# Kernel optimization log

Measured on AMD Instinct MI355X. Metric: run time of the kernel, lower is better.

The kernel has to match this reference:

```python
import jax, jax.numpy as jnp
import numpy as np

B, LQ, LK, D, NH = 16, 1024, 1024, 160, 8
HD = D // NH
EPS = 1e-5


def _ln(x, g, b):
    m = x.mean(-1, keepdims=True)
    v = ((x - m) ** 2).mean(-1, keepdims=True)
    return (x - m) / jnp.sqrt(v + EPS) * g + b


def _heads(x, L):
    # [B,L,D] -> [B,NH,L,HD]
    return x.reshape(B, L, NH, HD).transpose(0, 2, 1, 3)


def _attn(qh, kh, vh, scale):
    logits = jnp.einsum('bhqd,bhkd->bhqk', qh, kh) * scale
    p = jax.nn.softmax(logits, axis=-1)
    o = jnp.einsum('bhqk,bhkd->bhqd', p, vh)
    return o.transpose(0, 2, 1, 3).reshape(B, -1, D)


def setup_inputs() -> dict:
    key = jax.random.key(0)
    ks = jax.random.split(key, 16)
    s = 0.02
    inp = {
        'q': jax.random.normal(ks[0], (B, LQ, D), jnp.float32),
        'kv': jax.random.normal(ks[1], (B, LK, D), jnp.float32),
        'ln1_g': jnp.ones((D,), jnp.float32), 'ln1_b': jnp.zeros((D,), jnp.float32),
        'sa_in_w': jax.random.normal(ks[2], (3 * D, D), jnp.float32) * s,
        'sa_in_b': jnp.zeros((3 * D,), jnp.float32),
        'sa_out_w': jax.random.normal(ks[3], (D, D), jnp.float32) * s,
        'sa_out_b': jnp.zeros((D,), jnp.float32),
        'ln2_g': jnp.ones((D,), jnp.float32), 'ln2_b': jnp.zeros((D,), jnp.float32),
        'lnkv_g': jnp.ones((D,), jnp.float32), 'lnkv_b': jnp.zeros((D,), jnp.float32),
        'ca_qw': jax.random.normal(ks[4], (D, D), jnp.float32) * s,
        'ca_qb': jnp.zeros((D,), jnp.float32),
        'ca_kw': jax.random.normal(ks[5], (D, D), jnp.float32) * s,
        'ca_kb': jnp.zeros((D,), jnp.float32),
        'ca_vw': jax.random.normal(ks[6], (D, D), jnp.float32) * s,
        'ca_vb': jnp.zeros((D,), jnp.float32),
        'ca_ow': jax.random.normal(ks[7], (D, D), jnp.float32) * s,
        'ca_ob': jnp.zeros((D,), jnp.float32),
        'log_tau': jnp.zeros((1,), jnp.float32),
        'lnf_g': jnp.ones((D,), jnp.float32), 'lnf_b': jnp.zeros((D,), jnp.float32),
        'w1': jax.random.normal(ks[8], (4 * D, D), jnp.float32) * s,
        'b1': jnp.zeros((4 * D,), jnp.float32),
        'w2': jax.random.normal(ks[9], (D, 4 * D), jnp.float32) * s,
        'b2': jnp.zeros((D,), jnp.float32),
    }
    return inp


def reference(q, kv, ln1_g, ln1_b, sa_in_w, sa_in_b, sa_out_w, sa_out_b,
              ln2_g, ln2_b, lnkv_g, lnkv_b, ca_qw, ca_qb, ca_kw, ca_kb,
              ca_vw, ca_vb, ca_ow, ca_ob, log_tau, lnf_g, lnf_b,
              w1, b1, w2, b2):
    # --- self-attention (pre-LN), standard 1/sqrt(hd) scale ---
    qn = _ln(q, ln1_g, ln1_b)
    qkv = qn @ sa_in_w.T + sa_in_b  # [B,LQ,3D]
    sq, sk, sv = jnp.split(qkv, 3, axis=-1)
    sa = _attn(_heads(sq, LQ), _heads(sk, LQ), _heads(sv, LQ), HD ** -0.5)
    sa = sa @ sa_out_w.T + sa_out_b
    q = q + sa  # DropPath is identity in eval

    # --- cross-attention with learnable temperature ---
    qn = _ln(q, ln2_g, ln2_b)
    kvn = _ln(kv, lnkv_g, lnkv_b)
    tau = jnp.minimum(jax.nn.softplus(log_tau) + 0.5, 2.0)  # clamp max=2.0
    scale = (HD ** -0.5) / tau[0]
    qh = _heads(qn @ ca_qw.T + ca_qb, LQ)
    kh = _heads(kvn @ ca_kw.T + ca_kb, LK)
    vh = _heads(kvn @ ca_vw.T + ca_vb, LK)
    ca = _attn(qh, kh, vh, scale) @ ca_ow.T + ca_ob
    q = q + ca

    # --- FFN with exact GELU ---
    h = _ln(q, lnf_g, lnf_b) @ w1.T + b1
    h = jax.nn.gelu(h, approximate=False)
    q = q + (h @ w2.T + b2)
    return q
```

## Files before the change

### kernel.cpp

```cpp
#include <hip/hip_runtime.h>
#include <hip/hip_bf16.h>
#include <math.h>

#define LQN 1024
#define LKN 1024
#define NB 16
#define DM 160
#define NHEADS 8
#define HDIM 20

typedef __attribute__((ext_vector_type(8))) short bf16x8;
typedef __attribute__((ext_vector_type(4))) float f32x4;

__device__ __forceinline__ float bf2f(unsigned short h) {
  union { unsigned int u; float f; } c; c.u = ((unsigned int)h) << 16; return c.f;
}
__device__ __forceinline__ unsigned short f2bf(float f) {
  union { float f; unsigned int u; } c; c.f = f;
  unsigned int lsb = (c.u >> 16) & 1u;
  unsigned int r = c.u + 0x7fffu + lsb;
  return (unsigned short)(r >> 16);
}
__device__ __forceinline__ unsigned int cvtpk(float a, float b) {
  unsigned int r;
  asm("v_cvt_pk_bf16_f32 %0, %1, %2" : "=v"(r) : "v"(a), "v"(b));
  return r;
}
__device__ __forceinline__ float ex2(float x) { return __builtin_amdgcn_exp2f(x); }

__global__ void zero_kernel(uint4* __restrict__ p, int n4) {
  int i = blockIdx.x * 256 + threadIdx.x;
  if (i < n4) p[i] = make_uint4(0, 0, 0, 0);
}

__global__ void vinit_kernel(uint4* __restrict__ p, int n4) {
  int i = blockIdx.x * 256 + threadIdx.x;
  if (i < n4) {
    unsigned int v = ((i & 31) == 20) ? 0x3F803F80u : 0u;
    p[i] = make_uint4(v, v, v, v);
  }
}

struct CvtArgs {
  const float* src[8];
  int cum[9];
};
__global__ void cvt8_kernel(CvtArgs a, unsigned short* __restrict__ dst) {
  int i = blockIdx.x * 256 + threadIdx.x;
  if (i >= 409600) return;
  int s = 0;
#pragma unroll
  for (int t = 0; t < 7; ++t) s += (i >= a.cum[t + 1]) ? 1 : 0;
  dst[i] = f2bf(a.src[s][i - a.cum[s]]);
}

__global__ void ln_kernel(const float* __restrict__ x,
                          const float* __restrict__ g,
                          const float* __restrict__ b,
                          unsigned short* __restrict__ y, int rows) {
  int row = blockIdx.x * 4 + (threadIdx.x >> 6);
  int lane = threadIdx.x & 63;
  const float* xr = x + (size_t)row * DM;
  float a0 = xr[lane];
  float a1 = xr[lane + 64];
  float a2 = (lane < 32) ? xr[lane + 128] : 0.0f;
  float s = a0 + a1 + a2;
#pragma unroll
  for (int m = 1; m < 64; m <<= 1) s += __shfl_xor(s, m);
  float mean = s * (1.0f / DM);
  float d0 = a0 - mean, d1 = a1 - mean, d2 = a2 - mean;
  float vs = d0 * d0 + d1 * d1 + ((lane < 32) ? d2 * d2 : 0.0f);
#pragma unroll
  for (int m = 1; m < 64; m <<= 1) vs += __shfl_xor(vs, m);
  float rstd = rsqrtf(vs * (1.0f / DM) + 1e-5f);
  unsigned short* yr = y + (size_t)row * DM;
  yr[lane]      = f2bf(d0 * rstd * g[lane]      + b[lane]);
  yr[lane + 64] = f2bf(d1 * rstd * g[lane + 64] + b[lane + 64]);
  if (lane < 32)
    yr[lane + 128] = f2bf(d2 * rstd * g[lane + 128] + b[lane + 128]);
}

__global__ __launch_bounds__(256, 4)
void qkv_kernel(const unsigned short* __restrict__ Aq,
                const unsigned short* __restrict__ Akv,
                const unsigned short* __restrict__ Wq,
                const unsigned short* __restrict__ Wk,
                const unsigned short* __restrict__ Wv,
                const float* __restrict__ bq,
                const float* __restrict__ bk,
                const float* __restrict__ bv,
                unsigned short* __restrict__ Qp,
                unsigned short* __restrict__ Kc,
                unsigned short* __restrict__ Vc) {
  int which = blockIdx.y / 3;
  int yt = blockIdx.y % 3;
  const unsigned short* A = (which == 0) ? Aq : Akv;
  const unsigned short* W = (which == 0) ? Wq : (which == 1 ? Wk : Wv);
  const float* bias = (which == 0) ? bq : (which == 1 ? bk : bv);
  int lane = threadIdx.x & 63;
  int wid = threadIdx.x >> 6;
  int wr = wid >> 1, wc = wid & 1;
  int r0 = blockIdx.x * 64 + wr * 32;
  int c0 = yt * 64 + wc * 32;
  if (c0 >= 160) return;
  int lr = lane & 15;
  int ko = (lane >> 4) * 8;
  const unsigned short* Ap0 = A + (size_t)(r0 + lr) * 160 + ko;
  const unsigned short* Ap1 = Ap0 + (size_t)16 * 160;
  const unsigned short* Wp0 = W + (size_t)(c0 + lr) * 160 + ko;
  const unsigned short* Wp1 = Wp0 + (size_t)16 * 160;
  f32x4 acc00 = {0, 0, 0, 0}, acc01 = {0, 0, 0, 0};
  f32x4 acc10 = {0, 0, 0, 0}, acc11 = {0, 0, 0, 0};
#pragma unroll
  for (int k = 0; k < 160; k += 32) {
    bf16x8 a0 = *(const bf16x8*)(Ap0 + k);
    bf16x8 a1 = *(const bf16x8*)(Ap1 + k);
    bf16x8 b0 = *(const bf16x8*)(Wp0 + k);
    bf16x8 b1 = *(const bf16x8*)(Wp1 + k);
    acc00 = __builtin_amdgcn_mfma_f32_16x16x32_bf16(a0, b0, acc00, 0, 0, 0);
    acc01 = __builtin_amdgcn_mfma_f32_16x16x32_bf16(a0, b1, acc01, 0, 0, 0);
    acc10 = __builtin_amdgcn_mfma_f32_16x16x32_bf16(a1, b0, acc10, 0, 0, 0);
    acc11 = __builtin_amdgcn_mfma_f32_16x16x32_bf16(a1, b1, acc11, 0, 0, 0);
  }
  int cA = c0 + lr, cB = c0 + 16 + lr;
  float bc0 = bias[cA];
  float bc1 = bias[cB];
  int rb = (lane >> 4) * 4;
  int b = r0 >> 10;
  int hA = cA / 20, dA = cA % 20;
  int hB = cB / 20, dB = cB % 20;
  if (which == 0) {
    int pcA = hA * 32 + dA, pcB = hB * 32 + dB;
#pragma unroll
    for (int i = 0; i < 2; ++i) {
      f32x4 aA = i ? acc10 : acc00;
      f32x4 aB = i ? acc11 : acc01;
#pragma unroll
      for (int r = 0; r < 4; ++r) {
        int row = r0 + i * 16 + rb + r;
        Qp[(size_t)row * 256 + pcA] = f2bf(aA[r] + bc0);
        Qp[(size_t)row * 256 + pcB] = f2bf(aB[r] + bc1);
      }
    }
  } else if (which == 1) {
    size_t baseA = ((((size_t)(b * 8 + hA)) * 4 + (dA >> 3)) * 1024) * 8 + (dA & 7);
    size_t baseB = ((((size_t)(b * 8 + hB)) * 4 + (dB >> 3)) * 1024) * 8 + (dB & 7);
#pragma unroll
    for (int i = 0; i < 2; ++i) {
      f32x4 aA = i ? acc10 : acc00;
      f32x4 aB = i ? acc11 : acc01;
#pragma unroll
      for (int r = 0; r < 4; ++r) {
        int tok = (r0 & 1023) + i * 16 + rb + r;
        Kc[baseA + (size_t)tok * 8] = f2bf(aA[r] + bc0);
        Kc[baseB + (size_t)tok * 8] = f2bf(aB[r] + bc1);
      }
    }
  } else {
    int base64 = (r0 & 1023) & ~63;
    int hb = (r0 >> 5) & 1;
    int g = rb >> 2;
    size_t vbA = (((size_t)(b * 8 + hA) * 128 + (base64 >> 3)) * 32 + dA) * 8;
    size_t vbB = (((size_t)(b * 8 + hB) * 128 + (base64 >> 3)) * 32 + dB) * 8;
#pragma unroll
    for (int i = 0; i < 2; ++i) {
      f32x4 aA = i ? acc10 : acc00;
      f32x4 aB = i ? acc11 : acc01;
#pragma unroll
      for (int j = 0; j < 4; ++j) {
        size_t off = (size_t)(g + hb * 4) * 256 + i * 4 + j;
        Vc[vbA + off] = f2bf(aA[j] + bc0);
        Vc[vbB + off] = f2bf(aB[j] + bc1);
      }
    }
  }
}

template <int EPI, int K>
__global__ __launch_bounds__(256, 4)
void gemm_kernel(const unsigned short* __restrict__ A,
                 const unsigned short* __restrict__ W,
                 const float* __restrict__ bias,
                 const float* __restrict__ res,
                 void* __restrict__ outp, int N) {
  int lane = threadIdx.x & 63;
  int wid = threadIdx.x >> 6;
  int wr = wid >> 1, wc = wid & 1;
  int r0 = blockIdx.x * 64 + wr * 32;
  int c0 = blockIdx.y * 64 + wc * 32;
  if (c0 >= N) return;
  int lr = lane & 15;
  int ko = (lane >> 4) * 8;
  const unsigned short* Ap0 = A + (size_t)(r0 + lr) * K + ko;
  const unsigned short* Ap1 = Ap0 + (size_t)16 * K;
  const unsigned short* Wp0 = W + (size_t)(c0 + lr) * K + ko;
  const unsigned short* Wp1 = Wp0 + (size_t)16 * K;
  f32x4 acc00 = {0, 0, 0, 0}, acc01 = {0, 0, 0, 0};
  f32x4 acc10 = {0, 0, 0, 0}, acc11 = {0, 0, 0, 0};
#pragma unroll
  for (int k = 0; k < K; k += 32) {
    bf16x8 a0 = *(const bf16x8*)(Ap0 + k);
    bf16x8 a1 = *(const bf16x8*)(Ap1 + k);
    bf16x8 b0 = *(const bf16x8*)(Wp0 + k);
    bf16x8 b1 = *(const bf16x8*)(Wp1 + k);
    acc00 = __builtin_amdgcn_mfma_f32_16x16x32_bf16(a0, b0, acc00, 0, 0, 0);
    acc01 = __builtin_amdgcn_mfma_f32_16x16x32_bf16(a0, b1, acc01, 0, 0, 0);
    acc10 = __builtin_amdgcn_mfma_f32_16x16x32_bf16(a1, b0, acc10, 0, 0, 0);
    acc11 = __builtin_amdgcn_mfma_f32_16x16x32_bf16(a1, b1, acc11, 0, 0, 0);
  }
  int cA = c0 + lr, cB = c0 + 16 + lr;
  float bc0 = bias[cA];
  float bc1 = bias[cB];
  int rb = (lane >> 4) * 4;
#pragma unroll
  for (int i = 0; i < 2; ++i) {
    f32x4 aA = i ? acc10 : acc00;
    f32x4 aB = i ? acc11 : acc01;
#pragma unroll
    for (int r = 0; r < 4; ++r) {
      int row = r0 + i * 16 + rb + r;
      float v0 = aA[r] + bc0;
      float v1 = aB[r] + bc1;
      if (EPI == 2) {
        v0 = 0.5f * v0 * (1.0f + erff(v0 * 0.70710678118654752f));
        v1 = 0.5f * v1 * (1.0f + erff(v1 * 0.70710678118654752f));
        unsigned short* out = (unsigned short*)outp;
        out[(size_t)row * N + cA] = f2bf(v0);
        out[(size_t)row * N + cB] = f2bf(v1);
      } else {
        float* out = (float*)outp;
        out[(size_t)row * N + cA] = v0 + res[(size_t)row * N + cA];
        out[(size_t)row * N + cB] = v1 + res[(size_t)row * N + cB];
      }
    }
  }
}

__global__ __launch_bounds__(256, 4)
void attn_kernel(const unsigned short* __restrict__ Qp,
                 const unsigned short* __restrict__ Kc,
                 const unsigned short* __restrict__ Vc,
                 unsigned short* __restrict__ O,
                 const float* __restrict__ tau_ptr,
                 float base_scale) {
  __shared__ unsigned short kbuf[2][2048];
  __shared__ unsigned short vbuf[2][2048];
  int lane = threadIdx.x & 63;
  int wid = threadIdx.x >> 6;
  int bh = blockIdx.x;
  int b = bh >> 3, h = bh & 7;
  int q0 = blockIdx.y * 128 + wid * 32;
  float sc = base_scale;
  if (tau_ptr) {
    float lt = tau_ptr[0];
    float sp = (lt > 20.0f) ? lt : log1pf(expf(lt));
    sc /= fminf(sp + 0.5f, 2.0f);
  }
  float scale = sc * 1.4426950408889634f;
  int lr = lane & 15;
  int g = lane >> 4;
  int ko = g * 8;
  int rb = g * 4;
  const size_t tb = (size_t)b * LQN;
  union { bf16x8 v; unsigned short s[8]; unsigned int u[4]; } fq0, fq1;
  fq0.v = *(const bf16x8*)(Qp + (tb + q0 + lr) * 256 + h * 32 + ko);
  fq1.v = *(const bf16x8*)(Qp + (tb + q0 + 16 + lr) * 256 + h * 32 + ko);
#pragma unroll
  for (int j = 0; j < 4; ++j) {
    fq0.u[j] = cvtpk(bf2f(fq0.s[2 * j]) * scale, bf2f(fq0.s[2 * j + 1]) * scale);
    fq1.u[j] = cvtpk(bf2f(fq1.s[2 * j]) * scale, bf2f(fq1.s[2 * j + 1]) * scale);
  }
  bf16x8 aq0 = fq0.v, aq1 = fq1.v;
  const unsigned short* ksrc = Kc + (((size_t)bh * 4 + wid) * 1024) * 8;
  const unsigned short* vsrc = Vc + (size_t)bh * 32768;
  int sdst = wid * 512 + lane * 8;
  {
    uint4 k0 = *(const uint4*)(ksrc + lane * 8);
    uint4 v0 = *(const uint4*)(vsrc + sdst);
    *(uint4*)(kbuf[0] + sdst) = k0;
    *(uint4*)(vbuf[0] + sdst) = v0;
  }
  __syncthreads();
  int cur = 0;
  f32x4 o00 = {0, 0, 0, 0}, o01 = {0, 0, 0, 0};
  f32x4 o10 = {0, 0, 0, 0}, o11 = {0, 0, 0, 0};
  const f32x4 zero = {0, 0, 0, 0};
  for (int kt = 0; kt < LKN; kt += 64) {
    int ktn = (kt + 64 < LKN) ? kt + 64 : 0;
    uint4 kn = *(const uint4*)(ksrc + (ktn + lane) * 8);
    uint4 vn = *(const uint4*)(vsrc + ktn * 32 + sdst);
    const unsigned short* kb = kbuf[cur];
    const unsigned short* vbp = vbuf[cur];
    bf16x8 ck0 = *(const bf16x8*)(kb + g * 512 + lr * 8);
    bf16x8 ck1 = *(const bf16x8*)(kb + g * 512 + (16 + lr) * 8);
    bf16x8 ck2 = *(const bf16x8*)(kb + g * 512 + (32 + lr) * 8);
    bf16x8 ck3 = *(const bf16x8*)(kb + g * 512 + (48 + lr) * 8);
    f32x4 s0 = __builtin_amdgcn_mfma_f32_16x16x32_bf16(ck0, aq0, zero, 0, 0, 0);
    f32x4 s1 = __builtin_amdgcn_mfma_f32_16x16x32_bf16(ck1, aq0, zero, 0, 0, 0);
    f32x4 s2 = __builtin_amdgcn_mfma_f32_16x16x32_bf16(ck2, aq0, zero, 0, 0, 0);
    f32x4 s3 = __builtin_amdgcn_mfma_f32_16x16x32_bf16(ck3, aq0, zero, 0, 0, 0);
    union { bf16x8 v; unsigned int u[4]; } palo1, palo2, pahi1, pahi2;
    palo1.u[0] = cvtpk(ex2(s0[0]), ex2(s0[1]));
    palo1.u[1] = cvtpk(ex2(s0[2]), ex2(s0[3]));
    palo1.u[2] = cvtpk(ex2(s1[0]), ex2(s1[1]));
    palo1.u[3] = cvtpk(ex2(s1[2]), ex2(s1[3]));
    palo2.u[0] = cvtpk(ex2(s2[0]), ex2(s2[1]));
    palo2.u[1] = cvtpk(ex2(s2[2]), ex2(s2[3]));
    palo2.u[2] = cvtpk(ex2(s3[0]), ex2(s3[1]));
    palo2.u[3] = cvtpk(ex2(s3[2]), ex2(s3[3]));
    s0 = __builtin_amdgcn_mfma_f32_16x16x32_bf16(ck0, aq1, zero, 0, 0, 0);
    s1 = __builtin_amdgcn_mfma_f32_16x16x32_bf16(ck1, aq1, zero, 0, 0, 0);
    s2 = __builtin_amdgcn_mfma_f32_16x16x32_bf16(ck2, aq1, zero, 0, 0, 0);
    s3 = __builtin_amdgcn_mfma_f32_16x16x32_bf16(ck3, aq1, zero, 0, 0, 0);
    pahi1.u[0] = cvtpk(ex2(s0[0]), ex2(s0[1]));
    pahi1.u[1] = cvtpk(ex2(s0[2]), ex2(s0[3]));
    pahi1.u[2] = cvtpk(ex2(s1[0]), ex2(s1[1]));
    pahi1.u[3] = cvtpk(ex2(s1[2]), ex2(s1[3]));
    pahi2.u[0] = cvtpk(ex2(s2[0]), ex2(s2[1]));
    pahi2.u[1] = cvtpk(ex2(s2[2]), ex2(s2[3]));
    pahi2.u[2] = cvtpk(ex2(s3[0]), ex2(s3[1]));
    pahi2.u[3] = cvtpk(ex2(s3[2]), ex2(s3[3]));
    bf16x8 vb00 = *(const bf16x8*)(vbp + g * 256 + lr * 8);
    bf16x8 vb01 = *(const bf16x8*)(vbp + (4 + g) * 256 + lr * 8);
    bf16x8 vb10 = *(const bf16x8*)(vbp + g * 256 + (16 + lr) * 8);
    bf16x8 vb11 = *(const bf16x8*)(vbp + (4 + g) * 256 + (16 + lr) * 8);
    o00 = __builtin_amdgcn_mfma_f32_16x16x32_bf16(palo1.v, vb00, o00, 0, 0, 0);
    o00 = __builtin_amdgcn_mfma_f32_16x16x32_bf16(palo2.v, vb01, o00, 0, 0, 0);
    o01 = __builtin_amdgcn_mfma_f32_16x16x32_bf16(palo1.v, vb10, o01, 0, 0, 0);
    o01 = __builtin_amdgcn_mfma_f32_16x16x32_bf16(palo2.v, vb11, o01, 0, 0, 0);
    o10 = __builtin_amdgcn_mfma_f32_16x16x32_bf16(pahi1.v, vb00, o10, 0, 0, 0);
    o10 = __builtin_amdgcn_mfma_f32_16x16x32_bf16(pahi2.v, vb01, o10, 0, 0, 0);
    o11 = __builtin_amdgcn_mfma_f32_16x16x32_bf16(pahi1.v, vb10, o11, 0, 0, 0);
    o11 = __builtin_amdgcn_mfma_f32_16x16x32_bf16(pahi2.v, vb11, o11, 0, 0, 0);
    *(uint4*)(kbuf[cur ^ 1] + sdst) = kn;
    *(uint4*)(vbuf[cur ^ 1] + sdst) = vn;
    __syncthreads();
    cur ^= 1;
  }
  unsigned short* ob = O + (tb + q0) * DM + h * HDIM;
  int psl = (lane & 48) + 4;
#pragma unroll
  for (int r = 0; r < 4; ++r) {
    int qr = rb + r;
    float inv0 = 1.0f / __shfl(o01[r], psl, 64);
    ob[(size_t)qr * DM + lr] = f2bf(o00[r] * inv0);
    if (lr < 4) ob[(size_t)qr * DM + 16 + lr] = f2bf(o01[r] * inv0);
    float inv1 = 1.0f / __shfl(o11[r], psl, 64);
    ob[(size_t)(16 + qr) * DM + lr] = f2bf(o10[r] * inv1);
    if (lr < 4) ob[(size_t)(16 + qr) * DM + 16 + lr] = f2bf(o11[r] * inv1);
  }
}

extern "C" void kernel_launch(void* const* d_in, const int* in_sizes, int n_in,
                              void* d_out, int out_size, void* d_ws, size_t ws_size,
                              hipStream_t stream) {
  (void)in_sizes; (void)n_in; (void)out_size; (void)ws_size;
  const float* q        = (const float*)d_in[0];
  const float* kv       = (const float*)d_in[1];
  const float* ln1_g    = (const float*)d_in[2];
  const float* ln1_b    = (const float*)d_in[3];
  const float* sa_in_w  = (const float*)d_in[4];
  const float* sa_in_b  = (const float*)d_in[5];
  const float* sa_out_w = (const float*)d_in[6];
  const float* sa_out_b = (const float*)d_in[7];
  const float* ln2_g    = (const float*)d_in[8];
  const float* ln2_b    = (const float*)d_in[9];
  const float* lnkv_g   = (const float*)d_in[10];
  const float* lnkv_b   = (const float*)d_in[11];
  const float* ca_qw    = (const float*)d_in[12];
  const float* ca_qb    = (const float*)d_in[13];
  const float* ca_kw    = (const float*)d_in[14];
  const float* ca_kb    = (const float*)d_in[15];
  const float* ca_vw    = (const float*)d_in[16];
  const float* ca_vb    = (const float*)d_in[17];
  const float* ca_ow    = (const float*)d_in[18];
  const float* ca_ob    = (const float*)d_in[19];
  const float* log_tau  = (const float*)d_in[20];
  const float* lnf_g    = (const float*)d_in[21];
  const float* lnf_b    = (const float*)d_in[22];
  const float* w1       = (const float*)d_in[23];
  const float* b1       = (const float*)d_in[24];
  const float* w2       = (const float*)d_in[25];
  const float* b2       = (const float*)d_in[26];

  const int M = NB * LQN;
  char* ws = (char*)d_ws;
  unsigned short* wb   = (unsigned short*)(ws);
  unsigned short* qn   = (unsigned short*)(ws + 1048576);
  unsigned short* sqp  = (unsigned short*)(ws + 6291456);
  unsigned short* skc  = (unsigned short*)(ws + 14680064);
  unsigned short* svc  = (unsigned short*)(ws + 23068672);
  unsigned short* attn = (unsigned short*)(ws + 31457280);
  unsigned short* kvn  = (unsigned short*)(ws + 36700160);
  float*          q1   = (float*)(ws + 41943040);
  float*          q2   = (float*)(ws + 52428800);
  unsigned short* hbuf = (unsigned short*)(ws + 6291456);

  unsigned short* b_sa_in  = wb;
  unsigned short* b_sa_out = wb + 76800;
  unsigned short* b_ca_q   = wb + 102400;
  unsigned short* b_ca_k   = wb + 128000;
  unsigned short* b_ca_v   = wb + 153600;
  unsigned short* b_ca_o   = wb + 179200;
  unsigned short* b_w1     = wb + 204800;
  unsigned short* b_w2     = wb + 307200;

  dim3 blk(256);
  const float isq = 0.22360679774997896f;

  zero_kernel<<<dim3(4096), blk, 0, stream>>>((uint4*)(ws + 6291456), 1048576);
  vinit_kernel<<<dim3(2048), blk, 0, stream>>>((uint4*)(ws + 23068672), 524288);

  CvtArgs ca;
  ca.src[0] = sa_in_w;  ca.src[1] = sa_out_w; ca.src[2] = ca_qw; ca.src[3] = ca_kw;
  ca.src[4] = ca_vw;    ca.src[5] = ca_ow;    ca.src[6] = w1;    ca.src[7] = w2;
  int cum[9] = {0, 76800, 102400, 128000, 153600, 179200, 204800, 307200, 409600};
  for (int i = 0; i < 9; ++i) ca.cum[i] = cum[i];
  cvt8_kernel<<<dim3(1600), blk, 0, stream>>>(ca, wb);

  ln_kernel<<<dim3(M / 4), blk, 0, stream>>>(q, ln1_g, ln1_b, qn, M);
  qkv_kernel<<<dim3(M / 64, 9), blk, 0, stream>>>(
      qn, qn, b_sa_in, b_sa_in + 160 * 160, b_sa_in + 320 * 160,
      sa_in_b, sa_in_b + 160, sa_in_b + 320, sqp, skc, svc);
  attn_kernel<<<dim3(NB * NHEADS, LQN / 128), blk, 0, stream>>>(sqp, skc, svc, attn, nullptr, isq);
  gemm_kernel<1, 160><<<dim3(M / 64, 3), blk, 0, stream>>>(attn, b_sa_out, sa_out_b, q, q1, 160);

  ln_kernel<<<dim3(M / 4), blk, 0, stream>>>(q1, ln2_g, ln2_b, qn, M);
  ln_kernel<<<dim3(M / 4), blk, 0, stream>>>(kv, lnkv_g, lnkv_b, kvn, M);
  qkv_kernel<<<dim3(M / 64, 9), blk, 0, stream>>>(
      qn, kvn, b_ca_q, b_ca_k, b_ca_v,
      ca_qb, ca_kb, ca_vb, sqp, skc, svc);
  attn_kernel<<<dim3(NB * NHEADS, LQN / 128), blk, 0, stream>>>(sqp, skc, svc, attn, log_tau, isq);
  gemm_kernel<1, 160><<<dim3(M / 64, 3), blk, 0, stream>>>(attn, b_ca_o, ca_ob, q1, q2, 160);

  ln_kernel<<<dim3(M / 4), blk, 0, stream>>>(q2, lnf_g, lnf_b, qn, M);
  gemm_kernel<2, 160><<<dim3(M / 64, 10), blk, 0, stream>>>(qn, b_w1, b1, nullptr, hbuf, 640);
  gemm_kernel<1, 640><<<dim3(M / 64, 3), blk, 0, stream>>>(hbuf, b_w2, b2, q2, (float*)d_out, 160);
}
```

Measured before the change: 180.3 us.

## Stage full 160-column weight tile in LDS and compute all N columns per block

Replaces the 64x64-tile QKV and K=160 GEMM kernels with a gemm160 kernel. Each block loads a full 160x160 bf16 weight slab into padded shared memory, and each wave computes 16 rows across all 160 columns (10 MFMA accumulators). This removes the wasted third column tile (c0>=160 early return), cuts redundant global weight loads, and reduces the grid size. It also merges the zero/vinit kernels and concatenates the cross-attention biases so one launch covers Q, K and V. In exchange, the kernel uses about 53KB of LDS and more registers, with occupancy lowered to 2 blocks per CU.

```diff
diff --git a/kernel.cpp b/kernel.cpp
--- a/kernel.cpp
+++ b/kernel.cpp
@@ -28,17 +28,19 @@
 }
 __device__ __forceinline__ float ex2(float x) { return __builtin_amdgcn_exp2f(x); }
 
-__global__ void zero_kernel(uint4* __restrict__ p, int n4) {
+__global__ void init_kernel(uint4* __restrict__ zbase, int nz,
+                            uint4* __restrict__ vbase, int nv,
+                            const float* __restrict__ b0,
+                            const float* __restrict__ b1,
+                            const float* __restrict__ b2,
+                            float* __restrict__ bcat) {
   int i = blockIdx.x * 256 + threadIdx.x;
-  if (i < n4) p[i] = make_uint4(0, 0, 0, 0);
-}
-
-__global__ void vinit_kernel(uint4* __restrict__ p, int n4) {
-  int i = blockIdx.x * 256 + threadIdx.x;
-  if (i < n4) {
+  if (i < nz) zbase[i] = make_uint4(0, 0, 0, 0);
+  if (i < nv) {
     unsigned int v = ((i & 31) == 20) ? 0x3F803F80u : 0u;
-    p[i] = make_uint4(v, v, v, v);
-  }
+    vbase[i] = make_uint4(v, v, v, v);
+  }
+  if (i < 480) bcat[i] = (i < 160) ? b0[i] : (i < 320 ? b1[i - 160] : b2[i - 320]);
 }
 
 struct CvtArgs {
@@ -80,109 +82,131 @@
     yr[lane + 128] = f2bf(d2 * rstd * g[lane + 128] + b[lane + 128]);
 }
 
-__global__ __launch_bounds__(256, 4)
-void qkv_kernel(const unsigned short* __restrict__ Aq,
-                const unsigned short* __restrict__ Akv,
-                const unsigned short* __restrict__ Wq,
-                const unsigned short* __restrict__ Wk,
-                const unsigned short* __restrict__ Wv,
-                const float* __restrict__ bq,
-                const float* __restrict__ bk,
-                const float* __restrict__ bv,
-                unsigned short* __restrict__ Qp,
-                unsigned short* __restrict__ Kc,
-                unsigned short* __restrict__ Vc) {
-  int which = blockIdx.y / 3;
-  int yt = blockIdx.y % 3;
-  const unsigned short* A = (which == 0) ? Aq : Akv;
-  const unsigned short* W = (which == 0) ? Wq : (which == 1 ? Wk : Wv);
-  const float* bias = (which == 0) ? bq : (which == 1 ? bk : bv);
-  int lane = threadIdx.x & 63;
-  int wid = threadIdx.x >> 6;
-  int wr = wid >> 1, wc = wid & 1;
-  int r0 = blockIdx.x * 64 + wr * 32;
-  int c0 = yt * 64 + wc * 32;
-  if (c0 >= 160) return;
+template <int EPI>
+__global__ __launch_bounds__(256, 2)
+void gemm160_kernel(const unsigned short* __restrict__ Aq,
+                    const unsigned short* __restrict__ Akv,
+                    const unsigned short* __restrict__ W,
+                    const float* __restrict__ bias,
+                    const float* __restrict__ res,
+                    void* __restrict__ outp,
+                    unsigned short* __restrict__ Kc,
+                    unsigned short* __restrict__ Vc) {
+  __shared__ unsigned short wl[160 * 168];
+  int tid = threadIdx.x;
+  int lane = tid & 63;
+  int w = tid >> 6;
+  int y = blockIdx.y;
+  const unsigned short* Wb = W + y * 25600;
+#pragma unroll
+  for (int p = 0; p < 13; ++p) {
+    int idx = p * 2048 + tid * 8;
+    if (idx < 25600) {
+      int col = idx / 160, k = idx % 160;
+      *(uint4*)(wl + col * 168 + k) = *(const uint4*)(Wb + idx);
+    }
+  }
+  __syncthreads();
   int lr = lane & 15;
-  int ko = (lane >> 4) * 8;
-  const unsigned short* Ap0 = A + (size_t)(r0 + lr) * 160 + ko;
-  const unsigned short* Ap1 = Ap0 + (size_t)16 * 160;
-  const unsigned short* Wp0 = W + (size_t)(c0 + lr) * 160 + ko;
-  const unsigned short* Wp1 = Wp0 + (size_t)16 * 160;
-  f32x4 acc00 = {0, 0, 0, 0}, acc01 = {0, 0, 0, 0};
-  f32x4 acc10 = {0, 0, 0, 0}, acc11 = {0, 0, 0, 0};
-#pragma unroll
-  for (int k = 0; k < 160; k += 32) {
-    bf16x8 a0 = *(const bf16x8*)(Ap0 + k);
-    bf16x8 a1 = *(const bf16x8*)(Ap1 + k);
-    bf16x8 b0 = *(const bf16x8*)(Wp0 + k);
-    bf16x8 b1 = *(const bf16x8*)(Wp1 + k);
-    acc00 = __builtin_amdgcn_mfma_f32_16x16x32_bf16(a0, b0, acc00, 0, 0, 0);
-    acc01 = __builtin_amdgcn_mfma_f32_16x16x32_bf16(a0, b1, acc01, 0, 0, 0);
-    acc10 = __builtin_amdgcn_mfma_f32_16x16x32_bf16(a1, b0, acc10, 0, 0, 0);
-    acc11 = __builtin_amdgcn_mfma_f32_16x16x32_bf16(a1, b1, acc11, 0, 0, 0);
-  }
-  int cA = c0 + lr, cB = c0 + 16 + lr;
-  float bc0 = bias[cA];
-  float bc1 = bias[cB];
-  int rb = (lane >> 4) * 4;
-  int b = r0 >> 10;
-  int hA = cA / 20, dA = cA % 20;
-  int hB = cB / 20, dB = cB % 20;
-  if (which == 0) {
-    int pcA = hA * 32 + dA, pcB = hB * 32 + dB;
-#pragma unroll
-    for (int i = 0; i < 2; ++i) {
-      f32x4 aA = i ? acc10 : acc00;
-      f32x4 aB = i ? acc11 : acc01;
+  int g = lane >> 4;
+  int R0 = blockIdx.x * 64;
+  int rbase = R0 + w * 16;
+  const unsigned short* A = (EPI == 0 && y > 0) ? Akv : Aq;
+  const unsigned short* Ap = A + (size_t)(rbase + lr) * 160 + g * 8;
+  const unsigned short* wp = wl + lr * 168 + g * 8;
+  f32x4 acc[10];
+#pragma unroll
+  for (int c = 0; c < 10; ++c) acc[c] = (f32x4){0, 0, 0, 0};
+#pragma unroll
+  for (int k0 = 0; k0 < 160; k0 += 32) {
+    bf16x8 a = *(const bf16x8*)(Ap + k0);
+#pragma unroll
+    for (int c = 0; c < 10; ++c) {
+      bf16x8 bfr = *(const bf16x8*)(wp + c * 16 * 168 + k0);
+      acc[c] = __builtin_amdgcn_mfma_f32_16x16x32_bf16(a, bfr, acc[c], 0, 0, 0);
+    }
+  }
+  if (EPI == 0) {
+    if (y == 0) {
+      unsigned short* Qp = (unsigned short*)outp;
+#pragma unroll
+      for (int c = 0; c < 10; ++c) {
+        int col = c * 16 + lr;
+        int h = col / 20, d = col % 20;
+        float bc = bias[col];
+#pragma unroll
+        for (int r = 0; r < 4; ++r) {
+          int row = rbase + g * 4 + r;
+          Qp[(size_t)row * 256 + h * 32 + d] = f2bf(acc[c][r] + bc);
+        }
+      }
+    } else if (y == 1) {
+      int b = R0 >> 10;
+#pragma unroll
+      for (int c = 0; c < 10; ++c) {
+        int col = c * 16 + lr;
+        int h = col / 20, d = col % 20;
+        float bc = bias[160 + col];
+        size_t base = ((((size_t)(b * 8 + h)) * 4 + (d >> 3)) * 1024) * 8 + (d & 7);
+#pragma unroll
+        for (int r = 0; r < 4; ++r) {
+          int tok = (rbase + g * 4 + r) & 1023;
+          Kc[base + (size_t)tok * 8] = f2bf(acc[c][r] + bc);
+        }
+      }
+    } else {
+      int b = R0 >> 10;
+      int base64 = R0 & 1023;
+      int slotbase = base64 + g * 8 + (w & 1) * 4 + (w >> 1) * 32;
+#pragma unroll
+      for (int c = 0; c < 10; ++c) {
+        int col = c * 16 + lr;
+        int h = col / 20, d = col % 20;
+        float bc = bias[320 + col];
+        size_t vb = ((size_t)(b * 8 + h) * 128) * 256 + (size_t)d * 8;
+#pragma unroll
+        for (int r = 0; r < 4; ++r) {
+          int S = slotbase + r;
+          Vc[vb + (size_t)(S >> 3) * 256 + (S & 7)] = f2bf(acc[c][r] + bc);
+        }
+      }
+    }
+  } else if (EPI == 1) {
+    float* out = (float*)outp;
+#pragma unroll
+    for (int c = 0; c < 10; ++c) {
+      int col = c * 16 + lr;
+      float bc = bias[col];
 #pragma unroll
       for (int r = 0; r < 4; ++r) {
-        int row = r0 + i * 16 + rb + r;
-        Qp[(size_t)row * 256 + pcA] = f2bf(aA[r] + bc0);
-        Qp[(size_t)row * 256 + pcB] = f2bf(aB[r] + bc1);
+        int row = rbase + g * 4 + r;
+        out[(size_t)row * 160 + col] = acc[c][r] + bc + res[(size_t)row * 160 + col];
       }
     }
-  } else if (which == 1) {
-    size_t baseA = ((((size_t)(b * 8 + hA)) * 4 + (dA >> 3)) * 1024) * 8 + (dA & 7);
-    size_t baseB = ((((size_t)(b * 8 + hB)) * 4 + (dB >> 3)) * 1024) * 8 + (dB & 7);
-#pragma unroll
-    for (int i = 0; i < 2; ++i) {
-      f32x4 aA = i ? acc10 : acc00;
-      f32x4 aB = i ? acc11 : acc01;
+  } else {
+    unsigned short* out = (unsigned short*)outp;
+#pragma unroll
+    for (int c = 0; c < 10; ++c) {
+      int colg = y * 160 + c * 16 + lr;
+      float bc = bias[colg];
 #pragma unroll
       for (int r = 0; r < 4; ++r) {
-        int tok = (r0 & 1023) + i * 16 + rb + r;
-        Kc[baseA + (size_t)tok * 8] = f2bf(aA[r] + bc0);
-        Kc[baseB + (size_t)tok * 8] = f2bf(aB[r] + bc1);
+        int row = rbase + g * 4 + r;
+        float v = acc[c][r] + bc;
+        v = 0.5f * v * (1.0f + erff(v * 0.70710678118654752f));
+        out[(size_t)row * 640 + colg] = f2bf(v);
       }
     }
-  } else {
-    int base64 = (r0 & 1023) & ~63;
-    int hb = (r0 >> 5) & 1;
-    int g = rb >> 2;
-    size_t vbA = (((size_t)(b * 8 + hA) * 128 + (base64 >> 3)) * 32 + dA) * 8;
-    size_t vbB = (((size_t)(b * 8 + hB) * 128 + (base64 >> 3)) * 32 + dB) * 8;
-#pragma unroll
-    for (int i = 0; i < 2; ++i) {
-      f32x4 aA = i ? acc10 : acc00;
-      f32x4 aB = i ? acc11 : acc01;
-#pragma unroll
-      for (int j = 0; j < 4; ++j) {
-        size_t off = (size_t)(g + hb * 4) * 256 + i * 4 + j;
-        Vc[vbA + off] = f2bf(aA[j] + bc0);
-        Vc[vbB + off] = f2bf(aB[j] + bc1);
-      }
-    }
-  }
-}
-
-template <int EPI, int K>
+  }
+}
+
+template <int K>
 __global__ __launch_bounds__(256, 4)
 void gemm_kernel(const unsigned short* __restrict__ A,
                  const unsigned short* __restrict__ W,
                  const float* __restrict__ bias,
                  const float* __restrict__ res,
-                 void* __restrict__ outp, int N) {
+                 float* __restrict__ out, int N) {
   int lane = threadIdx.x & 63;
   int wid = threadIdx.x >> 6;
   int wr = wid >> 1, wc = wid & 1;
@@ -219,19 +243,8 @@
 #pragma unroll
     for (int r = 0; r < 4; ++r) {
       int row = r0 + i * 16 + rb + r;
-      float v0 = aA[r] + bc0;
-      float v1 = aB[r] + bc1;
-      if (EPI == 2) {
-        v0 = 0.5f * v0 * (1.0f + erff(v0 * 0.70710678118654752f));
-        v1 = 0.5f * v1 * (1.0f + erff(v1 * 0.70710678118654752f));
-        unsigned short* out = (unsigned short*)outp;
-        out[(size_t)row * N + cA] = f2bf(v0);
-        out[(size_t)row * N + cB] = f2bf(v1);
-      } else {
-        float* out = (float*)outp;
-        out[(size_t)row * N + cA] = v0 + res[(size_t)row * N + cA];
-        out[(size_t)row * N + cB] = v1 + res[(size_t)row * N + cB];
-      }
+      out[(size_t)row * N + cA] = aA[r] + bc0 + res[(size_t)row * N + cA];
+      out[(size_t)row * N + cB] = aB[r] + bc1 + res[(size_t)row * N + cB];
     }
   }
 }
@@ -386,6 +399,7 @@
   const int M = NB * LQN;
   char* ws = (char*)d_ws;
   unsigned short* wb   = (unsigned short*)(ws);
+  float*          bcat = (float*)(ws + 860160);
   unsigned short* qn   = (unsigned short*)(ws + 1048576);
   unsigned short* sqp  = (unsigned short*)(ws + 6291456);
   unsigned short* skc  = (unsigned short*)(ws + 14680064);
@@ -399,8 +413,6 @@
   unsigned short* b_sa_in  = wb;
   unsigned short* b_sa_out = wb + 76800;
   unsigned short* b_ca_q   = wb + 102400;
-  unsigned short* b_ca_k   = wb + 128000;
-  unsigned short* b_ca_v   = wb + 153600;
   unsigned short* b_ca_o   = wb + 179200;
   unsigned short* b_w1     = wb + 204800;
   unsigned short* b_w2     = wb + 307200;
@@ -408,8 +420,9 @@
   dim3 blk(256);
   const float isq = 0.22360679774997896f;
 
-  zero_kernel<<<dim3(4096), blk, 0, stream>>>((uint4*)(ws + 6291456), 1048576);
-  vinit_kernel<<<dim3(2048), blk, 0, stream>>>((uint4*)(ws + 23068672), 524288);
+  init_kernel<<<dim3(4096), blk, 0, stream>>>(
+      (uint4*)(ws + 6291456), 1048576, (uint4*)(ws + 23068672), 524288,
+      ca_qb, ca_kb, ca_vb, bcat);
 
   CvtArgs ca;
   ca.src[0] = sa_in_w;  ca.src[1] = sa_out_w; ca.src[2] = ca_qw; ca.src[3] = ca_kw;
@@ -419,21 +432,22 @@
   cvt8_kernel<<<dim3(1600), blk, 0, stream>>>(ca, wb);
 
   ln_kernel<<<dim3(M / 4), blk, 0, stream>>>(q, ln1_g, ln1_b, qn, M);
-  qkv_kernel<<<dim3(M / 64, 9), blk, 0, stream>>>(
-      qn, qn, b_sa_in, b_sa_in + 160 * 160, b_sa_in + 320 * 160,
-      sa_in_b, sa_in_b + 160, sa_in_b + 320, sqp, skc, svc);
+  gemm160_kernel<0><<<dim3(M / 64, 3), blk, 0, stream>>>(
+      qn, qn, b_sa_in, sa_in_b, nullptr, sqp, skc, svc);
   attn_kernel<<<dim3(NB * NHEADS, LQN / 128), blk, 0, stream>>>(sqp, skc, svc, attn, nullptr, isq);
-  gemm_kernel<1, 160><<<dim3(M / 64, 3), blk, 0, stream>>>(attn, b_sa_out, sa_out_b, q, q1, 160);
+  gemm160_kernel<1><<<dim3(M / 64, 1), blk, 0, stream>>>(
+      attn, attn, b_sa_out, sa_out_b, q, q1, nullptr, nullptr);
 
   ln_kernel<<<dim3(M / 4), blk, 0, stream>>>(q1, ln2_g, ln2_b, qn, M);
   ln_kernel<<<dim3(M / 4), blk, 0, stream>>>(kv, lnkv_g, lnkv_b, kvn, M);
-  qkv_kernel<<<dim3(M / 64, 9), blk, 0, stream>>>(
-      qn, kvn, b_ca_q, b_ca_k, b_ca_v,
-      ca_qb, ca_kb, ca_vb, sqp, skc, svc);
+  gemm160_kernel<0><<<dim3(M / 64, 3), blk, 0, stream>>>(
+      qn, kvn, b_ca_q, bcat, nullptr, sqp, skc, svc);
   attn_kernel<<<dim3(NB * NHEADS, LQN / 128), blk, 0, stream>>>(sqp, skc, svc, attn, log_tau, isq);
-  gemm_kernel<1, 160><<<dim3(M / 64, 3), blk, 0, stream>>>(attn, b_ca_o, ca_ob, q1, q2, 160);
+  gemm160_kernel<1><<<dim3(M / 64, 1), blk, 0, stream>>>(
+      attn, attn, b_ca_o, ca_ob, q1, q2, nullptr, nullptr);
 
   ln_kernel<<<dim3(M / 4), blk, 0, stream>>>(q2, lnf_g, lnf_b, qn, M);
-  gemm_kernel<2, 160><<<dim3(M / 64, 10), blk, 0, stream>>>(qn, b_w1, b1, nullptr, hbuf, 640);
-  gemm_kernel<1, 640><<<dim3(M / 64, 3), blk, 0, stream>>>(hbuf, b_w2, b2, q2, (float*)d_out, 160);
-}
+  gemm160_kernel<2><<<dim3(M / 64, 4), blk, 0, stream>>>(
+      qn, qn, b_w1, b1, nullptr, hbuf, nullptr, nullptr);
+  gemm_kernel<640><<<dim3(M / 64, 3), blk, 0, stream>>>(hbuf, b_w2, b2, q2, (float*)d_out, 160);
+}
```

Measured after the change: 175.8 us. -2.5%, faster.
